# Kernel tuning notes

Measured on AMD Instinct MI355X. Metric: run time of the kernel, lower is better.

The kernel has to match this reference:

```python
import jax, jax.numpy as jnp
import numpy as np

# Model dims (match init_kwargs cfg)
B, C_IN, L = 16, 3, 1024
D_MODEL, N_LAYERS = 256, 4
D_STATE, D_CONV, EXPAND = 16, 4, 2
D_INNER = EXPAND * D_MODEL            # 512
DT_RANK = (D_MODEL + 15) // 16        # 16 (mamba_ssm 'auto' rank)


def setup_inputs() -> dict:
    key = jax.random.key(0)
    ks = jax.random.split(key, 10)
    def rn(k, shape, scale):
        return jax.random.normal(k, shape, jnp.float32) * scale
    inp = {
        "x": jax.random.normal(ks[0], (B, C_IN, L), jnp.float32),
        # input stem: Conv1d(3 -> d_model, k=3, pad=1)
        "stem_w": rn(ks[1], (D_MODEL, C_IN, 3), 0.3),
        "stem_b": jnp.zeros((D_MODEL,), jnp.float32),
        # per-layer params, stacked on leading layer dim
        "norm_g": jnp.ones((N_LAYERS, D_MODEL), jnp.float32),
        "norm_b": jnp.zeros((N_LAYERS, D_MODEL), jnp.float32),
        "in_proj_w": rn(ks[2], (N_LAYERS, 2 * D_INNER, D_MODEL), 0.02),
        "conv_w": rn(ks[3], (N_LAYERS, D_INNER, D_CONV), 0.2),
        "conv_b": jnp.zeros((N_LAYERS, D_INNER), jnp.float32),
        "x_proj_w": rn(ks[4], (N_LAYERS, DT_RANK + 2 * D_STATE, D_INNER), 0.02),
        "dt_w": rn(ks[5], (N_LAYERS, D_INNER, DT_RANK), 0.05),
        "dt_b": jnp.full((N_LAYERS, D_INNER), -4.6, jnp.float32),  # softplus ~= 0.01
        "A_log": jnp.log(jnp.broadcast_to(
            jnp.arange(1, D_STATE + 1, dtype=jnp.float32), (N_LAYERS, D_INNER, D_STATE))),
        "Dp": jnp.ones((N_LAYERS, D_INNER), jnp.float32),
        "out_w": rn(ks[6], (N_LAYERS, D_MODEL, D_INNER), 0.02),
        # final norm + output head Conv1d(d_model -> 1, k=1)
        "fnorm_g": jnp.ones((D_MODEL,), jnp.float32),
        "fnorm_b": jnp.zeros((D_MODEL,), jnp.float32),
        "head_w": rn(ks[7], (1, D_MODEL), 0.05),
        "head_b": jnp.zeros((1,), jnp.float32),
    }
    return inp


def _layernorm(x, g, b, eps=1e-5):
    mu = jnp.mean(x, axis=-1, keepdims=True)
    var = jnp.mean((x - mu) ** 2, axis=-1, keepdims=True)
    return (x - mu) * jax.lax.rsqrt(var + eps) * g + b


def _silu(x):
    return x * jax.nn.sigmoid(x)


def _selective_scan(u, delta, A, Bm, Cm, D):
    # u, delta: [B, L, di]; Bm, Cm: [B, L, ds]; A: [di, ds]; D: [di]
    # h_t = exp(delta_t * A) * h_{t-1} + (delta_t * u_t) * B_t ; y_t = <C_t, h_t>
    def step(h, t):
        d_t, B_t, C_t, u_t = t  # [B,di], [B,ds], [B,ds], [B,di]
        h = h * jnp.exp(d_t[..., None] * A) + (d_t * u_t)[..., None] * B_t[:, None, :]
        return h, jnp.einsum('bds,bs->bd', h, C_t)
    h0 = jnp.zeros((u.shape[0], A.shape[0], A.shape[1]), u.dtype)
    xs = (jnp.moveaxis(delta, 1, 0), jnp.moveaxis(Bm, 1, 0),
          jnp.moveaxis(Cm, 1, 0), jnp.moveaxis(u, 1, 0))
    _, ys = jax.lax.scan(step, h0, xs)            # ys: [L, B, di]
    return jnp.moveaxis(ys, 0, 1) + u * D


def _mamba(x, in_w, cw, cb, xw, dtw, dtb, A_log, Dp, ow):
    # x: [B, L, d_model]
    xz = jnp.einsum('bld,ed->ble', x, in_w)       # [B, L, 2*di]
    xin, z = jnp.split(xz, 2, axis=-1)
    # causal depthwise conv over time
    xc = jnp.moveaxis(xin, 1, 2)                  # [B, di, L]
    xc = jax.lax.conv_general_dilated(
        xc, cw[:, None, :], (1,), [(D_CONV - 1, 0)],
        feature_group_count=D_INNER,
        dimension_numbers=('NCH', 'OIH', 'NCH')) + cb[None, :, None]
    xin = _silu(jnp.moveaxis(xc, 1, 2))           # [B, L, di]
    proj = jnp.einsum('bld,ed->ble', xin, xw)     # [B, L, dt_rank + 2*ds]
    dt = proj[..., :DT_RANK]
    Bm = proj[..., DT_RANK:DT_RANK + D_STATE]
    Cm = proj[..., DT_RANK + D_STATE:]
    delta = jax.nn.softplus(jnp.einsum('blr,dr->bld', dt, dtw) + dtb)
    A = -jnp.exp(A_log)
    y = _selective_scan(xin, delta, A, Bm, Cm, Dp)
    y = y * _silu(z)
    return jnp.einsum('bld,od->blo', y, ow)       # [B, L, d_model]


def reference(x, stem_w, stem_b, norm_g, norm_b, in_proj_w, conv_w, conv_b,
              x_proj_w, dt_w, dt_b, A_log, Dp, out_w, fnorm_g, fnorm_b,
              head_w, head_b):
    # stem: Conv1d(k=3, same padding) + ReLU
    h = jax.lax.conv_general_dilated(
        x, stem_w, (1,), [(1, 1)],
        dimension_numbers=('NCH', 'OIH', 'NCH')) + stem_b[None, :, None]
    h = jax.nn.relu(h)
    h = jnp.moveaxis(h, 1, 2)                     # [B, L, d_model]
    for i in range(N_LAYERS):
        h = h + _mamba(_layernorm(h, norm_g[i], norm_b[i]),
                       in_proj_w[i], conv_w[i], conv_b[i], x_proj_w[i],
                       dt_w[i], dt_b[i], A_log[i], Dp[i], out_w[i])
    h = _layernorm(h, fnorm_g, fnorm_b)
    out = jnp.einsum('bld,od->blo', h, head_w) + head_b
    return jax.nn.sigmoid(jnp.moveaxis(out, 1, 2))  # [B, 1, L]
```

## Files before the change

### kernel.cpp

```cpp
#include <hip/hip_runtime.h>
#include <math.h>

#define BSZ 16
#define LQ 1024
#define DM 256
#define DI 512
#define NT (BSZ*LQ)

typedef __attribute__((ext_vector_type(8))) short short8;
typedef __attribute__((ext_vector_type(4))) short short4v;
typedef __attribute__((ext_vector_type(4))) float f32x4;

#define AS1(p) (const __attribute__((address_space(1))) void*)(p)
#define AS3(p) (__attribute__((address_space(3))) void*)(p)
#define GLOAD16(g, l) __builtin_amdgcn_global_load_lds(AS1(g), AS3(l), 16, 0, 0)

__device__ __forceinline__ short f2bf(float f) {
  union { float f; unsigned u; } a; a.f = f;
  unsigned r = (a.u + 0x7FFF + ((a.u >> 16) & 1)) >> 16;
  return (short)r;
}
__device__ __forceinline__ float bf2f(short s) {
  union { unsigned u; float f; } a; a.u = ((unsigned)(unsigned short)s) << 16;
  return a.f;
}

__global__ void stem_kernel(const float* __restrict__ x, const float* __restrict__ w,
                            const float* __restrict__ bias, float* __restrict__ h) {
  int idx = blockIdx.x * 256 + threadIdx.x;
  int d = idx & 255;
  int l = (idx >> 8) & 1023;
  int b = idx >> 18;
  float acc = bias[d];
#pragma unroll
  for (int c = 0; c < 3; c++) {
    const float* xr = x + (size_t)(b * 3 + c) * LQ;
    const float* wr = w + (size_t)(d * 3 + c) * 3;
#pragma unroll
    for (int k = 0; k < 3; k++) {
      int t = l + k - 1;
      if (t >= 0 && t < LQ) acc += xr[t] * wr[k];
    }
  }
  h[idx] = fmaxf(acc, 0.f);
}

#define WB_IN 262144
#define WB_XP 32768
#define WB_OUT 131072
#define WB_L (WB_IN + WB_XP + WB_OUT)

__global__ void convert_w(const float* __restrict__ in_w, const float* __restrict__ xp_w,
                          const float* __restrict__ out_w, short* __restrict__ wb) {
  int layer = blockIdx.y;
  int idx = blockIdx.x * 256 + threadIdx.x;
  short* dst = wb + (size_t)layer * WB_L;
  float v;
  if (idx < WB_IN) {
    v = in_w[(size_t)layer * WB_IN + idx];
  } else if (idx < WB_IN + WB_XP) {
    int k = idx - WB_IN; int row = k >> 9, col = k & 511;
    v = (row < 48) ? xp_w[(size_t)layer * 48 * 512 + row * 512 + col] : 0.f;
  } else {
    int k = idx - WB_IN - WB_XP;
    v = out_w[(size_t)layer * WB_OUT + k];
  }
  dst[idx] = f2bf(v);
}

__global__ void ln_kernel(const float* __restrict__ x, const float* __restrict__ g,
                          const float* __restrict__ bv, short* __restrict__ o) {
  int token = blockIdx.x * 4 + (threadIdx.x >> 6);
  int lane = threadIdx.x & 63;
  f32x4 v = *(const f32x4*)(x + (size_t)token * DM + lane * 4);
  float s = v[0] + v[1] + v[2] + v[3];
  float q = v[0]*v[0] + v[1]*v[1] + v[2]*v[2] + v[3]*v[3];
#pragma unroll
  for (int off = 32; off > 0; off >>= 1) {
    s += __shfl_xor(s, off, 64);
    q += __shfl_xor(q, off, 64);
  }
  float mu = s * (1.f / DM);
  float var = q * (1.f / DM) - mu * mu;
  float rs = rsqrtf(var + 1e-5f);
  f32x4 gg = *(const f32x4*)(g + lane * 4);
  f32x4 bb = *(const f32x4*)(bv + lane * 4);
  short4v ov;
#pragma unroll
  for (int k = 0; k < 4; k++) ov[k] = f2bf((v[k] - mu) * rs * gg[k] + bb[k]);
  *(short4v*)(o + (size_t)token * DM + lane * 4) = ov;
}

__global__ __launch_bounds__(256) void gemm_mfma_s16(
    const short* __restrict__ A, int K,
    const short* __restrict__ W,
    short* __restrict__ C0, int ld0,
    short* __restrict__ C1, int ld1,
    int split, int N) {
  __shared__ short As[128 * 32];
  __shared__ short Bs[128 * 32];
  int tid = threadIdx.x;
  int wave = tid >> 6, lane = tid & 63;
  int bm = blockIdx.y * 128, bn = blockIdx.x * 128;
  int wm = (wave >> 1) * 64, wn = (wave & 1) * 64;

  f32x4 acc[4][4];
#pragma unroll
  for (int i = 0; i < 4; i++)
#pragma unroll
    for (int j = 0; j < 4; j++) { acc[i][j][0]=0.f; acc[i][j][1]=0.f; acc[i][j][2]=0.f; acc[i][j][3]=0.f; }

  int srow = lane >> 2;
  int scol = (lane & 3) * 8;
  const short* Ag = A + (size_t)(bm + wave * 32 + srow) * K + scol;
  const short* Wg = W + (size_t)(bn + wave * 32 + srow) * K + scol;
  short* AsW = As + wave * 32 * 32;
  short* BsW = Bs + wave * 32 * 32;

  int fr = lane & 15;
  int kg = (lane >> 4) * 8;

  for (int k0 = 0; k0 < K; k0 += 32) {
    GLOAD16(Ag + k0,                    AsW);
    GLOAD16(Ag + k0 + (size_t)16 * K,   AsW + 16 * 32);
    GLOAD16(Wg + k0,                    BsW);
    GLOAD16(Wg + k0 + (size_t)16 * K,   BsW + 16 * 32);
    __syncthreads();

    short8 af[4], bf[4];
#pragma unroll
    for (int i = 0; i < 4; i++) af[i] = *(const short8*)&As[(wm + i * 16 + fr) * 32 + kg];
#pragma unroll
    for (int j = 0; j < 4; j++) bf[j] = *(const short8*)&Bs[(wn + j * 16 + fr) * 32 + kg];
#pragma unroll
    for (int i = 0; i < 4; i++)
#pragma unroll
      for (int j = 0; j < 4; j++)
        acc[i][j] = __builtin_amdgcn_mfma_f32_16x16x32_bf16(af[i], bf[j], acc[i][j], 0, 0, 0);
    __syncthreads();
  }

  int cn = lane & 15, cr = (lane >> 4) * 4;
#pragma unroll
  for (int i = 0; i < 4; i++) {
    int row0 = bm + wm + i * 16 + cr;
#pragma unroll
    for (int j = 0; j < 4; j++) {
      int col = bn + wn + j * 16 + cn;
      if (col < N) {
#pragma unroll
        for (int r = 0; r < 4; r++) {
          short* p = (col < split) ? (C0 + (size_t)(row0 + r) * ld0 + col)
                                   : (C1 + (size_t)(row0 + r) * ld1 + (col - split));
          *p = f2bf(acc[i][j][r]);
        }
      }
    }
  }
}

__global__ __launch_bounds__(256) void gemm2_xproj(
    const short* __restrict__ A,
    const short* __restrict__ W,
    float* __restrict__ proj) {
  __shared__ short As[32 * 64];
  __shared__ short Bs[64 * 64];
  int tid = threadIdx.x;
  int wave = tid >> 6, lane = tid & 63;
  int bm = blockIdx.y * 32;
  int wm = (wave >> 1) * 16, wn = (wave & 1) * 32;

  f32x4 acc[2];
  acc[0] = (f32x4){0.f,0.f,0.f,0.f};
  acc[1] = (f32x4){0.f,0.f,0.f,0.f};

  int arow = tid >> 3, akk = (tid & 7) * 8;
  const short* Ag = A + (size_t)(bm + arow) * 512 + akk;
  int fr = lane & 15, kg = (lane >> 4) * 8;

  for (int k0 = 0; k0 < 512; k0 += 64) {
    GLOAD16(Ag + k0, As + tid * 8);
#pragma unroll
    for (int i = 0; i < 2; i++) {
      int c = tid + i * 256;
      int row = c >> 3, kk = (c & 7) * 8;
      GLOAD16(W + (size_t)row * 512 + k0 + kk, Bs + c * 8);
    }
    __syncthreads();

#pragma unroll
    for (int ks = 0; ks < 2; ks++) {
      short8 af = *(const short8*)&As[(wm + fr) * 64 + ks * 32 + kg];
#pragma unroll
      for (int j = 0; j < 2; j++) {
        short8 bf = *(const short8*)&Bs[(wn + j * 16 + fr) * 64 + ks * 32 + kg];
        acc[j] = __builtin_amdgcn_mfma_f32_16x16x32_bf16(af, bf, acc[j], 0, 0, 0);
      }
    }
    __syncthreads();
  }

  int cn = lane & 15, cr = (lane >> 4) * 4;
  int row0 = bm + wm + cr;
#pragma unroll
  for (int j = 0; j < 2; j++) {
    int col = wn + j * 16 + cn;
    if (col < 48) {
#pragma unroll
      for (int r = 0; r < 4; r++)
        proj[(size_t)(row0 + r) * 48 + col] = acc[j][r];
    }
  }
}

__global__ __launch_bounds__(256) void gemm_mfma64(
    const short* __restrict__ A, int K,
    const short* __restrict__ W,
    float* __restrict__ C, int ldc, int N, int accum) {
  __shared__ short As[64 * 64];
  __shared__ short Bs[64 * 64];
  int tid = threadIdx.x;
  int wave = tid >> 6, lane = tid & 63;
  int bm = blockIdx.y * 64, bn = blockIdx.x * 64;
  int wm = (wave >> 1) * 32, wn = (wave & 1) * 32;

  f32x4 acc[2][2];
#pragma unroll
  for (int i = 0; i < 2; i++)
#pragma unroll
    for (int j = 0; j < 2; j++) { acc[i][j][0]=0.f; acc[i][j][1]=0.f; acc[i][j][2]=0.f; acc[i][j][3]=0.f; }

  const short* Ag = A + (size_t)bm * K;
  const short* Wg = W + (size_t)bn * K;
  int fr = lane & 15;
  int kg = (lane >> 4) * 8;

  for (int k0 = 0; k0 < K; k0 += 64) {
#pragma unroll
    for (int i = 0; i < 2; i++) {
      int c = tid + i * 256;
      int row = c >> 3, kk = (c & 7) * 8;
      GLOAD16(Ag + (size_t)row * K + k0 + kk, As + c * 8);
      GLOAD16(Wg + (size_t)row * K + k0 + kk, Bs + c * 8);
    }
    __syncthreads();

#pragma unroll
    for (int ks = 0; ks < 2; ks++) {
      short8 af[2], bf[2];
#pragma unroll
      for (int i = 0; i < 2; i++) af[i] = *(const short8*)&As[(wm + i * 16 + fr) * 64 + ks * 32 + kg];
#pragma unroll
      for (int j = 0; j < 2; j++) bf[j] = *(const short8*)&Bs[(wn + j * 16 + fr) * 64 + ks * 32 + kg];
#pragma unroll
      for (int i = 0; i < 2; i++)
#pragma unroll
        for (int j = 0; j < 2; j++)
          acc[i][j] = __builtin_amdgcn_mfma_f32_16x16x32_bf16(af[i], bf[j], acc[i][j], 0, 0, 0);
    }
    __syncthreads();
  }

  int cn = lane & 15, cr = (lane >> 4) * 4;
#pragma unroll
  for (int i = 0; i < 2; i++) {
    int row0 = bm + wm + i * 16 + cr;
#pragma unroll
    for (int j = 0; j < 2; j++) {
      int col = bn + wn + j * 16 + cn;
      if (col < N) {
#pragma unroll
        for (int r = 0; r < 4; r++) {
          float v = acc[i][j][r];
          float* p = C + (size_t)(row0 + r) * ldc + col;
          if (accum) v += *p;
          *p = v;
        }
      }
    }
  }
}

__global__ void conv_silu_kernel(const short* __restrict__ xcb, const float* __restrict__ cw,
                                 const float* __restrict__ cb, short* __restrict__ xinb) {
  int idx = blockIdx.x * 256 + threadIdx.x;
  int d8 = (idx & 63) * 8;
  int l = (idx >> 6) & 1023;
  int b = idx >> 16;
  int t = b * 1024 + l;
  short8 xv[4];
#pragma unroll
  for (int k = 0; k < 4; k++) {
    if (l + k - 3 >= 0) xv[k] = *(const short8*)(xcb + (size_t)(t + k - 3) * 512 + d8);
    else xv[k] = (short8)0;
  }
  short8 ov;
#pragma unroll
  for (int e = 0; e < 8; e++) {
    f32x4 wv = *(const f32x4*)(cw + (d8 + e) * 4);
    float acc = cb[d8 + e];
#pragma unroll
    for (int k = 0; k < 4; k++) acc += bf2f(xv[k][e]) * wv[k];
    acc = acc / (1.f + __expf(-acc));
    ov[e] = f2bf(acc);
  }
  *(short8*)(xinb + (size_t)t * 512 + d8) = ov;
}

template <int CTRL>
__device__ __forceinline__ float dpp_add(float x) {
  int yi = __builtin_amdgcn_update_dpp(0, __float_as_int(x), CTRL, 0xF, 0xF, true);
  return x + __int_as_float(yi);
}
__device__ __forceinline__ float sum16(float x) {
  x = dpp_add<0xB1>(x);
  x = dpp_add<0x4E>(x);
  x = dpp_add<0x124>(x);
  x = dpp_add<0x128>(x);
  return x;
}

#define TCH 32
__global__ __launch_bounds__(256) void scan_kernel(
    const short* __restrict__ xinb, const float* __restrict__ proj,
    const short* __restrict__ zc,
    const float* __restrict__ dt_w, const float* __restrict__ dt_b,
    const float* __restrict__ A_log, const float* __restrict__ Dp,
    short* __restrict__ ybf) {
  int b  = blockIdx.x >> 5;
  int d0 = (blockIdx.x & 31) << 4;
  int tid = threadIdx.x;
  int ci = tid >> 4;
  int s  = tid & 15;
  int d = d0 + ci;

  __shared__ float sDt[32 * 20];
  __shared__ float sBT[16 * 36];
  __shared__ float sCT[16 * 36];
  __shared__ float sUT[16 * 36];
  __shared__ float sDU[16 * 36];
  __shared__ float sDel[16 * 36];
  __shared__ float sY[32 * 17];

  float Av = -__expf(A_log[(size_t)d * 16 + s]);
  f32x4 wv4[4];
#pragma unroll
  for (int k = 0; k < 4; k++) wv4[k] = *(const f32x4*)&dt_w[(size_t)d * 16 + k * 4];
  float db = dt_b[d];
  float Ddj = Dp[d0 + s];
  float h = 0.f;

  const float* projb = proj + (size_t)b * LQ * 48;
  const short* xinbb = xinb + (size_t)b * LQ * 512 + d0;
  const short* zcb   = zc   + (size_t)b * LQ * 512 + d0;
  short* ybb         = ybf  + (size_t)b * LQ * 512 + d0;

  int tt = tid >> 4, j = tid & 15;

  int tr[6], rr[6];
#pragma unroll
  for (int k = 0; k < 6; k++) { int idx = tid + k * 256; tr[k] = idx / 48; rr[k] = idx - tr[k] * 48; }

  float uv0, uv1, zv0, zv1;
  {
    float pjv[6];
#pragma unroll
    for (int k = 0; k < 6; k++) pjv[k] = projb[tid + k * 256];
    uv0 = bf2f(xinbb[(size_t)tt * 512 + j]);
    uv1 = bf2f(xinbb[(size_t)(tt + 16) * 512 + j]);
    zv0 = bf2f(zcb[(size_t)tt * 512 + j]);
    zv1 = bf2f(zcb[(size_t)(tt + 16) * 512 + j]);
#pragma unroll
    for (int k = 0; k < 6; k++) {
      int r = rr[k], t = tr[k];
      if (r < 16)      sDt[t * 20 + r] = pjv[k];
      else if (r < 32) sBT[(r - 16) * 36 + t] = pjv[k];
      else             sCT[(r - 32) * 36 + t] = pjv[k];
    }
    sUT[j * 36 + tt] = uv0;
    sUT[j * 36 + tt + 16] = uv1;
  }
  __syncthreads();

  const int NCH = LQ / TCH;
  for (int c = 0; c < NCH; c++) {
    int t0 = c * TCH;

    float pjn[6], un0 = 0.f, un1 = 0.f, zn0 = 0.f, zn1 = 0.f;
    if (c + 1 < NCH) {
      const float* g = projb + (t0 + TCH) * 48;
#pragma unroll
      for (int k = 0; k < 6; k++) pjn[k] = g[tid + k * 256];
      un0 = bf2f(xinbb[(size_t)(t0 + TCH + tt) * 512 + j]);
      un1 = bf2f(xinbb[(size_t)(t0 + TCH + tt + 16) * 512 + j]);
      zn0 = bf2f(zcb[(size_t)(t0 + TCH + tt) * 512 + j]);
      zn1 = bf2f(zcb[(size_t)(t0 + TCH + tt + 16) * 512 + j]);
    }

    {
      f32x4 a0 = *(const f32x4*)&sDt[s * 20 + 0];
      f32x4 a1 = *(const f32x4*)&sDt[s * 20 + 4];
      f32x4 a2 = *(const f32x4*)&sDt[s * 20 + 8];
      f32x4 a3 = *(const f32x4*)&sDt[s * 20 + 12];
      f32x4 b0 = *(const f32x4*)&sDt[(s + 16) * 20 + 0];
      f32x4 b1 = *(const f32x4*)&sDt[(s + 16) * 20 + 4];
      f32x4 b2 = *(const f32x4*)&sDt[(s + 16) * 20 + 8];
      f32x4 b3 = *(const f32x4*)&sDt[(s + 16) * 20 + 12];
      float dt0 = db, dt1 = db;
#pragma unroll
      for (int q = 0; q < 4; q++) {
        dt0 += a0[q] * wv4[0][q] + a1[q] * wv4[1][q] + a2[q] * wv4[2][q] + a3[q] * wv4[3][q];
        dt1 += b0[q] * wv4[0][q] + b1[q] * wv4[1][q] + b2[q] * wv4[2][q] + b3[q] * wv4[3][q];
      }
      float de0 = (dt0 > 15.f) ? dt0 : __logf(1.f + __expf(dt0));
      float de1 = (dt1 > 15.f) ? dt1 : __logf(1.f + __expf(dt1));
      float u0 = sUT[ci * 36 + s];
      float u1 = sUT[ci * 36 + s + 16];
      sDel[ci * 36 + s]      = de0;
      sDel[ci * 36 + s + 16] = de1;
      sDU[ci * 36 + s]       = de0 * u0;
      sDU[ci * 36 + s + 16]  = de1 * u1;
    }
    __syncthreads();

    {
      float ee[TCH], cin[TCH];
      f32x4 ct[8];
      {
        f32x4 dl[8], du8[8], bt[8];
#pragma unroll
        for (int k = 0; k < 8; k++) {
          dl[k]  = *(const f32x4*)&sDel[ci * 36 + k * 4];
          du8[k] = *(const f32x4*)&sDU[ci * 36 + k * 4];
          bt[k]  = *(const f32x4*)&sBT[s * 36 + k * 4];
          ct[k]  = *(const f32x4*)&sCT[s * 36 + k * 4];
        }
#pragma unroll
        for (int t = 0; t < TCH; t++) {
          ee[t] = __expf(dl[t >> 2][t & 3] * Av);
          cin[t] = du8[t >> 2][t & 3] * bt[t >> 2][t & 3];
        }
      }
      float pv0 = 0.f, pv1 = 0.f;
#pragma unroll
      for (int t = 0; t < TCH; t++) {
        h = h * ee[t] + cin[t];
        float p = sum16(h * ct[t >> 2][t & 3]);
        if (t < 16) pv0 = (s == t) ? p : pv0;
        else        pv1 = (s == (t - 16)) ? p : pv1;
      }
      sY[s * 17 + ci] = pv0;
      sY[(s + 16) * 17 + ci] = pv1;
    }
    __syncthreads();

    {
      float p0 = sY[tt * 17 + j];
      float p1 = sY[(tt + 16) * 17 + j];
      float y0 = p0 + uv0 * Ddj;
      float y1 = p1 + uv1 * Ddj;
      float g0 = zv0 / (1.f + __expf(-zv0));
      float g1 = zv1 / (1.f + __expf(-zv1));
      ybb[(size_t)(t0 + tt) * 512 + j] = f2bf(y0 * g0);
      ybb[(size_t)(t0 + tt + 16) * 512 + j] = f2bf(y1 * g1);
    }
    if (c + 1 < NCH) {
#pragma unroll
      for (int k = 0; k < 6; k++) {
        int r = rr[k], t = tr[k];
        if (r < 16)      sDt[t * 20 + r] = pjn[k];
        else if (r < 32) sBT[(r - 16) * 36 + t] = pjn[k];
        else             sCT[(r - 32) * 36 + t] = pjn[k];
      }
      sUT[j * 36 + tt] = un0;
      sUT[j * 36 + tt + 16] = un1;
      uv0 = un0; uv1 = un1; zv0 = zn0; zv1 = zn1;
    }
    __syncthreads();
  }
}

__global__ void head_kernel(const float* __restrict__ h, const float* __restrict__ g,
                            const float* __restrict__ bv, const float* __restrict__ hw,
                            const float* __restrict__ hb, float* __restrict__ out) {
  int token = blockIdx.x;
  int d = threadIdx.x;
  float v = h[(size_t)token * DM + d];
  float s = v, q = v * v;
#pragma unroll
  for (int off = 32; off > 0; off >>= 1) {
    s += __shfl_down(s, off, 64);
    q += __shfl_down(q, off, 64);
  }
  __shared__ float ss[4], qq[4], cc[4];
  int lane = d & 63, wid = d >> 6;
  if (lane == 0) { ss[wid] = s; qq[wid] = q; }
  __syncthreads();
  s = ss[0] + ss[1] + ss[2] + ss[3];
  q = qq[0] + qq[1] + qq[2] + qq[3];
  float mu = s * (1.f / DM);
  float var = q * (1.f / DM) - mu * mu;
  float rs = rsqrtf(var + 1e-5f);
  float xn = (v - mu) * rs * g[d] + bv[d];
  float c = xn * hw[d];
#pragma unroll
  for (int off = 32; off > 0; off >>= 1) c += __shfl_down(c, off, 64);
  if (lane == 0) cc[wid] = c;
  __syncthreads();
  if (threadIdx.x == 0) {
    float t = cc[0] + cc[1] + cc[2] + cc[3] + hb[0];
    out[token] = 1.f / (1.f + __expf(-t));
  }
}

extern "C" void kernel_launch(void* const* d_in, const int* in_sizes, int n_in,
                              void* d_out, int out_size, void* d_ws, size_t ws_size,
                              hipStream_t stream) {
  const float* x        = (const float*)d_in[0];
  const float* stem_w   = (const float*)d_in[1];
  const float* stem_b   = (const float*)d_in[2];
  const float* norm_g   = (const float*)d_in[3];
  const float* norm_b   = (const float*)d_in[4];
  const float* in_proj_w= (const float*)d_in[5];
  const float* conv_w   = (const float*)d_in[6];
  const float* conv_b   = (const float*)d_in[7];
  const float* x_proj_w = (const float*)d_in[8];
  const float* dt_w     = (const float*)d_in[9];
  const float* dt_b     = (const float*)d_in[10];
  const float* A_log    = (const float*)d_in[11];
  const float* Dp       = (const float*)d_in[12];
  const float* out_w    = (const float*)d_in[13];
  const float* fnorm_g  = (const float*)d_in[14];
  const float* fnorm_b  = (const float*)d_in[15];
  const float* head_w   = (const float*)d_in[16];
  const float* head_b   = (const float*)d_in[17];

  char* base = (char*)d_ws;
  float* h    = (float*)(base);
  short* xcb  = (short*)(base + ((size_t)16 << 20));
  short* zcb  = (short*)(base + ((size_t)32 << 20));
  short* xnb  = (short*)(base + ((size_t)48 << 20));
  short* xinb = (short*)(base + ((size_t)56 << 20));
  short* ybf  = (short*)(base + ((size_t)72 << 20));
  float* proj = (float*)(base + ((size_t)88 << 20));
  short* wb   = (short*)(base + ((size_t)91 << 20));

  stem_kernel<<<NT, 256, 0, stream>>>(x, stem_w, stem_b, h);

  dim3 gcw(WB_L / 256, 4);
  convert_w<<<gcw, 256, 0, stream>>>(in_proj_w, x_proj_w, out_w, wb);

  for (int i = 0; i < 4; i++) {
    const short* wbl = wb + (size_t)i * WB_L;

    ln_kernel<<<NT / 4, 256, 0, stream>>>(h, norm_g + i * DM, norm_b + i * DM, xnb);

    dim3 g1(8, NT / 128);
    gemm_mfma_s16<<<g1, 256, 0, stream>>>(xnb, 256, wbl, xcb, 512, zcb, 512, 512, 1024);

    conv_silu_kernel<<<NT * DI / (256 * 8), 256, 0, stream>>>(xcb, conv_w + i * DI * 4,
                                                              conv_b + i * DI, xinb);

    dim3 g2(1, NT / 32);
    gemm2_xproj<<<g2, 256, 0, stream>>>(xinb, wbl + WB_IN, proj);

    scan_kernel<<<512, 256, 0, stream>>>(xinb, proj, zcb,
                                         dt_w + (size_t)i * DI * 16, dt_b + i * DI,
                                         A_log + (size_t)i * DI * 16, Dp + i * DI, ybf);

    dim3 g3(4, NT / 64);
    gemm_mfma64<<<g3, 256, 0, stream>>>(ybf, 512, wbl + WB_IN + WB_XP, h, 256, 256, 1);
  }

  head_kernel<<<NT, 256, 0, stream>>>(h, fnorm_g, fnorm_b, head_w, head_b, (float*)d_out);
}
```

Measured before the change: 794.6 us.

## Double GEMM K-step per barrier and widen scan time chunks to 64

The GEMM now loads two 32-wide K slices into separate LDS buffers per iteration and runs both MFMA sub-steps before one barrier pair, halving synchronization per K. The selective scan processes 64 timesteps per chunk instead of 32, computing the recurrence in two 32-step halves, which halves the chunk-loop barriers and prefetch rounds. This raises LDS use and register pressure (larger prefetch arrays), which may reduce occupancy.

After: 803.6 us. No clear change (+1.1%).

```diff
diff --git a/kernel.cpp b/kernel.cpp
--- a/kernel.cpp
+++ b/kernel.cpp
@@ -97,8 +97,8 @@
     short* __restrict__ C0, int ld0,
     short* __restrict__ C1, int ld1,
     int split, int N) {
-  __shared__ short As[128 * 32];
-  __shared__ short Bs[128 * 32];
+  __shared__ short As[2][128 * 32];
+  __shared__ short Bs[2][128 * 32];
   int tid = threadIdx.x;
   int wave = tid >> 6, lane = tid & 63;
   int bm = blockIdx.y * 128, bn = blockIdx.x * 128;
@@ -114,29 +114,38 @@
   int scol = (lane & 3) * 8;
   const short* Ag = A + (size_t)(bm + wave * 32 + srow) * K + scol;
   const short* Wg = W + (size_t)(bn + wave * 32 + srow) * K + scol;
-  short* AsW = As + wave * 32 * 32;
-  short* BsW = Bs + wave * 32 * 32;
+  short* As0W = As[0] + wave * 32 * 32;
+  short* As1W = As[1] + wave * 32 * 32;
+  short* Bs0W = Bs[0] + wave * 32 * 32;
+  short* Bs1W = Bs[1] + wave * 32 * 32;
 
   int fr = lane & 15;
   int kg = (lane >> 4) * 8;
 
-  for (int k0 = 0; k0 < K; k0 += 32) {
-    GLOAD16(Ag + k0,                    AsW);
-    GLOAD16(Ag + k0 + (size_t)16 * K,   AsW + 16 * 32);
-    GLOAD16(Wg + k0,                    BsW);
-    GLOAD16(Wg + k0 + (size_t)16 * K,   BsW + 16 * 32);
-    __syncthreads();
-
-    short8 af[4], bf[4];
-#pragma unroll
-    for (int i = 0; i < 4; i++) af[i] = *(const short8*)&As[(wm + i * 16 + fr) * 32 + kg];
-#pragma unroll
-    for (int j = 0; j < 4; j++) bf[j] = *(const short8*)&Bs[(wn + j * 16 + fr) * 32 + kg];
-#pragma unroll
-    for (int i = 0; i < 4; i++)
-#pragma unroll
-      for (int j = 0; j < 4; j++)
-        acc[i][j] = __builtin_amdgcn_mfma_f32_16x16x32_bf16(af[i], bf[j], acc[i][j], 0, 0, 0);
+  for (int k0 = 0; k0 < K; k0 += 64) {
+    GLOAD16(Ag + k0,                         As0W);
+    GLOAD16(Ag + k0 + (size_t)16 * K,        As0W + 16 * 32);
+    GLOAD16(Ag + k0 + 32,                    As1W);
+    GLOAD16(Ag + k0 + 32 + (size_t)16 * K,   As1W + 16 * 32);
+    GLOAD16(Wg + k0,                         Bs0W);
+    GLOAD16(Wg + k0 + (size_t)16 * K,        Bs0W + 16 * 32);
+    GLOAD16(Wg + k0 + 32,                    Bs1W);
+    GLOAD16(Wg + k0 + 32 + (size_t)16 * K,   Bs1W + 16 * 32);
+    __syncthreads();
+
+#pragma unroll
+    for (int ks = 0; ks < 2; ks++) {
+      short8 af[4], bf[4];
+#pragma unroll
+      for (int i = 0; i < 4; i++) af[i] = *(const short8*)&As[ks][(wm + i * 16 + fr) * 32 + kg];
+#pragma unroll
+      for (int j = 0; j < 4; j++) bf[j] = *(const short8*)&Bs[ks][(wn + j * 16 + fr) * 32 + kg];
+#pragma unroll
+      for (int i = 0; i < 4; i++)
+#pragma unroll
+        for (int j = 0; j < 4; j++)
+          acc[i][j] = __builtin_amdgcn_mfma_f32_16x16x32_bf16(af[i], bf[j], acc[i][j], 0, 0, 0);
+    }
     __syncthreads();
   }
 
@@ -320,7 +329,8 @@
   return x;
 }
 
-#define TCH 32
+#define TCH 64
+#define STT 68
 __global__ __launch_bounds__(256) void scan_kernel(
     const short* __restrict__ xinb, const float* __restrict__ proj,
     const short* __restrict__ zc,
@@ -334,13 +344,13 @@
   int s  = tid & 15;
   int d = d0 + ci;
 
-  __shared__ float sDt[32 * 20];
-  __shared__ float sBT[16 * 36];
-  __shared__ float sCT[16 * 36];
-  __shared__ float sUT[16 * 36];
-  __shared__ float sDU[16 * 36];
-  __shared__ float sDel[16 * 36];
-  __shared__ float sY[32 * 17];
+  __shared__ float sDt[64 * 20];
+  __shared__ float sBT[16 * STT];
+  __shared__ float sCT[16 * STT];
+  __shared__ float sUT[16 * STT];
+  __shared__ float sDU[16 * STT];
+  __shared__ float sDel[16 * STT];
+  __shared__ float sY[64 * 17];
 
   float Av = -__expf(A_log[(size_t)d * 16 + s]);
   f32x4 wv4[4];
@@ -357,28 +367,29 @@
 
   int tt = tid >> 4, j = tid & 15;
 
-  int tr[6], rr[6];
-#pragma unroll
-  for (int k = 0; k < 6; k++) { int idx = tid + k * 256; tr[k] = idx / 48; rr[k] = idx - tr[k] * 48; }
-
-  float uv0, uv1, zv0, zv1;
+  int tr[12], rr[12];
+#pragma unroll
+  for (int k = 0; k < 12; k++) { int idx = tid + k * 256; tr[k] = idx / 48; rr[k] = idx - tr[k] * 48; }
+
+  float uv[4], zv[4];
   {
-    float pjv[6];
-#pragma unroll
-    for (int k = 0; k < 6; k++) pjv[k] = projb[tid + k * 256];
-    uv0 = bf2f(xinbb[(size_t)tt * 512 + j]);
-    uv1 = bf2f(xinbb[(size_t)(tt + 16) * 512 + j]);
-    zv0 = bf2f(zcb[(size_t)tt * 512 + j]);
-    zv1 = bf2f(zcb[(size_t)(tt + 16) * 512 + j]);
-#pragma unroll
-    for (int k = 0; k < 6; k++) {
+    float pjv[12];
+#pragma unroll
+    for (int k = 0; k < 12; k++) pjv[k] = projb[tid + k * 256];
+#pragma unroll
+    for (int m = 0; m < 4; m++) {
+      uv[m] = bf2f(xinbb[(size_t)(tt + 16 * m) * 512 + j]);
+      zv[m] = bf2f(zcb[(size_t)(tt + 16 * m) * 512 + j]);
+    }
+#pragma unroll
+    for (int k = 0; k < 12; k++) {
       int r = rr[k], t = tr[k];
       if (r < 16)      sDt[t * 20 + r] = pjv[k];
-      else if (r < 32) sBT[(r - 16) * 36 + t] = pjv[k];
-      else             sCT[(r - 32) * 36 + t] = pjv[k];
-    }
-    sUT[j * 36 + tt] = uv0;
-    sUT[j * 36 + tt + 16] = uv1;
+      else if (r < 32) sBT[(r - 16) * STT + t] = pjv[k];
+      else             sCT[(r - 32) * STT + t] = pjv[k];
+    }
+#pragma unroll
+    for (int m = 0; m < 4; m++) sUT[j * STT + tt + 16 * m] = uv[m];
   }
   __syncthreads();
 
@@ -386,95 +397,89 @@
   for (int c = 0; c < NCH; c++) {
     int t0 = c * TCH;
 
-    float pjn[6], un0 = 0.f, un1 = 0.f, zn0 = 0.f, zn1 = 0.f;
+    float pjn[12], un[4], zn[4];
     if (c + 1 < NCH) {
       const float* g = projb + (t0 + TCH) * 48;
 #pragma unroll
-      for (int k = 0; k < 6; k++) pjn[k] = g[tid + k * 256];
-      un0 = bf2f(xinbb[(size_t)(t0 + TCH + tt) * 512 + j]);
-      un1 = bf2f(xinbb[(size_t)(t0 + TCH + tt + 16) * 512 + j]);
-      zn0 = bf2f(zcb[(size_t)(t0 + TCH + tt) * 512 + j]);
-      zn1 = bf2f(zcb[(size_t)(t0 + TCH + tt + 16) * 512 + j]);
-    }
-
-    {
-      f32x4 a0 = *(const f32x4*)&sDt[s * 20 + 0];
-      f32x4 a1 = *(const f32x4*)&sDt[s * 20 + 4];
-      f32x4 a2 = *(const f32x4*)&sDt[s * 20 + 8];
-      f32x4 a3 = *(const f32x4*)&sDt[s * 20 + 12];
-      f32x4 b0 = *(const f32x4*)&sDt[(s + 16) * 20 + 0];
-      f32x4 b1 = *(const f32x4*)&sDt[(s + 16) * 20 + 4];
-      f32x4 b2 = *(const f32x4*)&sDt[(s + 16) * 20 + 8];
-      f32x4 b3 = *(const f32x4*)&sDt[(s + 16) * 20 + 12];
-      float dt0 = db, dt1 = db;
-#pragma unroll
-      for (int q = 0; q < 4; q++) {
-        dt0 += a0[q] * wv4[0][q] + a1[q] * wv4[1][q] + a2[q] * wv4[2][q] + a3[q] * wv4[3][q];
-        dt1 += b0[q] * wv4[0][q] + b1[q] * wv4[1][q] + b2[q] * wv4[2][q] + b3[q] * wv4[3][q];
-      }
-      float de0 = (dt0 > 15.f) ? dt0 : __logf(1.f + __expf(dt0));
-      float de1 = (dt1 > 15.f) ? dt1 : __logf(1.f + __expf(dt1));
-      float u0 = sUT[ci * 36 + s];
-      float u1 = sUT[ci * 36 + s + 16];
-      sDel[ci * 36 + s]      = de0;
-      sDel[ci * 36 + s + 16] = de1;
-      sDU[ci * 36 + s]       = de0 * u0;
-      sDU[ci * 36 + s + 16]  = de1 * u1;
-    }
-    __syncthreads();
-
-    {
-      float ee[TCH], cin[TCH];
+      for (int k = 0; k < 12; k++) pjn[k] = g[tid + k * 256];
+#pragma unroll
+      for (int m = 0; m < 4; m++) {
+        un[m] = bf2f(xinbb[(size_t)(t0 + TCH + tt + 16 * m) * 512 + j]);
+        zn[m] = bf2f(zcb[(size_t)(t0 + TCH + tt + 16 * m) * 512 + j]);
+      }
+    }
+
+#pragma unroll
+    for (int m = 0; m < 4; m++) {
+      int st = s + 16 * m;
+      f32x4 r0 = *(const f32x4*)&sDt[st * 20 + 0];
+      f32x4 r1 = *(const f32x4*)&sDt[st * 20 + 4];
+      f32x4 r2 = *(const f32x4*)&sDt[st * 20 + 8];
+      f32x4 r3 = *(const f32x4*)&sDt[st * 20 + 12];
+      float dt = db;
+#pragma unroll
+      for (int q = 0; q < 4; q++)
+        dt += r0[q] * wv4[0][q] + r1[q] * wv4[1][q] + r2[q] * wv4[2][q] + r3[q] * wv4[3][q];
+      float de = (dt > 15.f) ? dt : __logf(1.f + __expf(dt));
+      float u = sUT[ci * STT + st];
+      sDel[ci * STT + st] = de;
+      sDU[ci * STT + st]  = de * u;
+    }
+    __syncthreads();
+
+#pragma unroll
+    for (int half = 0; half < 2; half++) {
+      int base = half * 32;
+      float ee[32], cin[32];
       f32x4 ct[8];
       {
         f32x4 dl[8], du8[8], bt[8];
 #pragma unroll
         for (int k = 0; k < 8; k++) {
-          dl[k]  = *(const f32x4*)&sDel[ci * 36 + k * 4];
-          du8[k] = *(const f32x4*)&sDU[ci * 36 + k * 4];
-          bt[k]  = *(const f32x4*)&sBT[s * 36 + k * 4];
-          ct[k]  = *(const f32x4*)&sCT[s * 36 + k * 4];
+          dl[k]  = *(const f32x4*)&sDel[ci * STT + base + k * 4];
+          du8[k] = *(const f32x4*)&sDU[ci * STT + base + k * 4];
+          bt[k]  = *(const f32x4*)&sBT[s * STT + base + k * 4];
+          ct[k]  = *(const f32x4*)&sCT[s * STT + base + k * 4];
         }
 #pragma unroll
-        for (int t = 0; t < TCH; t++) {
+        for (int t = 0; t < 32; t++) {
           ee[t] = __expf(dl[t >> 2][t & 3] * Av);
           cin[t] = du8[t >> 2][t & 3] * bt[t >> 2][t & 3];
         }
       }
       float pv0 = 0.f, pv1 = 0.f;
 #pragma unroll
-      for (int t = 0; t < TCH; t++) {
+      for (int t = 0; t < 32; t++) {
         h = h * ee[t] + cin[t];
         float p = sum16(h * ct[t >> 2][t & 3]);
         if (t < 16) pv0 = (s == t) ? p : pv0;
         else        pv1 = (s == (t - 16)) ? p : pv1;
       }
-      sY[s * 17 + ci] = pv0;
-      sY[(s + 16) * 17 + ci] = pv1;
-    }
-    __syncthreads();
-
-    {
-      float p0 = sY[tt * 17 + j];
-      float p1 = sY[(tt + 16) * 17 + j];
-      float y0 = p0 + uv0 * Ddj;
-      float y1 = p1 + uv1 * Ddj;
-      float g0 = zv0 / (1.f + __expf(-zv0));
-      float g1 = zv1 / (1.f + __expf(-zv1));
-      ybb[(size_t)(t0 + tt) * 512 + j] = f2bf(y0 * g0);
-      ybb[(size_t)(t0 + tt + 16) * 512 + j] = f2bf(y1 * g1);
+      sY[(base + s) * 17 + ci] = pv0;
+      sY[(base + s + 16) * 17 + ci] = pv1;
+    }
+    __syncthreads();
+
+#pragma unroll
+    for (int m = 0; m < 4; m++) {
+      float p = sY[(tt + 16 * m) * 17 + j];
+      float y = p + uv[m] * Ddj;
+      float g = zv[m] / (1.f + __expf(-zv[m]));
+      ybb[(size_t)(t0 + tt + 16 * m) * 512 + j] = f2bf(y * g);
     }
     if (c + 1 < NCH) {
 #pragma unroll
-      for (int k = 0; k < 6; k++) {
+      for (int k = 0; k < 12; k++) {
         int r = rr[k], t = tr[k];
         if (r < 16)      sDt[t * 20 + r] = pjn[k];
-        else if (r < 32) sBT[(r - 16) * 36 + t] = pjn[k];
-        else             sCT[(r - 32) * 36 + t] = pjn[k];
-      }
-      sUT[j * 36 + tt] = un0;
-      sUT[j * 36 + tt + 16] = un1;
-      uv0 = un0; uv1 = un1; zv0 = zn0; zv1 = zn1;
+        else if (r < 32) sBT[(r - 16) * STT + t] = pjn[k];
+        else             sCT[(r - 32) * STT + t] = pjn[k];
+      }
+#pragma unroll
+      for (int m = 0; m < 4; m++) {
+        sUT[j * STT + tt + 16 * m] = un[m];
+        uv[m] = un[m]; zv[m] = zn[m];
+      }
     }
     __syncthreads();
   }
```
